# Kernel tuning notes

Measured on AMD Instinct MI355X. Metric: run time of the kernel, lower is better.

The kernel has to match this reference:

```python
import jax, jax.numpy as jnp
import numpy as np

N_HEADS = 4
D_K = 64

def setup_inputs() -> dict:
    key = jax.random.key(0)
    k1, k2, k3 = jax.random.split(key, 3)
    B, C, H, W = 16, 256, 32, 32
    x = jax.random.normal(k1, (B, C, H, W), dtype=jnp.float32)
    # Linear(C, 3*n_heads*d_k) stored as [in, out] for x @ W
    w_proj = jax.random.normal(k2, (C, 3 * N_HEADS * D_K), dtype=jnp.float32) * (1.0 / np.sqrt(C))
    b_proj = jnp.zeros((3 * N_HEADS * D_K,), dtype=jnp.float32)
    w_out = jax.random.normal(k3, (N_HEADS * D_K, C), dtype=jnp.float32) * (1.0 / np.sqrt(N_HEADS * D_K))
    b_out = jnp.zeros((C,), dtype=jnp.float32)
    return {"x": x, "w_proj": w_proj, "b_proj": b_proj, "w_out": w_out, "b_out": b_out}

def reference(x, w_proj, b_proj, w_out, b_out):
    B, C, H, W = x.shape
    S = H * W
    scale = D_K ** -0.5
    xs = x.reshape(B, C, S).transpose(0, 2, 1)            # [B, S, C]
    qkv = (xs @ w_proj + b_proj).reshape(B, S, N_HEADS, 3 * D_K)
    q, k, v = jnp.split(qkv, 3, axis=3)                    # each [B, S, H, dk]
    attn = jnp.einsum('bihd,bjhd->bijh', q, k) * scale     # [B, S, S, heads]
    attn = jax.nn.softmax(attn, axis=2)
    o = jnp.einsum('bijh,bjhd->bihd', attn, v)             # [B, S, heads, dk]
    o = o.reshape(B, S, N_HEADS * D_K)
    res = o @ w_out + b_out + xs                           # [B, S, C]
    return res.transpose(0, 2, 1).reshape(B, C, H, W)
```

## Files before the change

### kernel.cpp

```cpp
#include <hip/hip_runtime.h>
#include <math.h>

#define B_  16
#define C_  256
#define S_  1024
#define NH  4
#define DK  64
#define P3  768
#define ND  256

typedef unsigned short u16;
typedef unsigned int   u32;
typedef float  f32x4  __attribute__((ext_vector_type(4)));
typedef short  bf16x8 __attribute__((ext_vector_type(8)));

#define MFMA16(a, b, c) __builtin_amdgcn_mfma_f32_16x16x32_bf16(a, b, c, 0, 0, 0)

#define QSCALE 0.1803368801111137f

__device__ __forceinline__ u16 f2bf(float f) {
    union { float f; u32 u; } x; x.f = f;
    u32 r = x.u + 0x7fffu + ((x.u >> 16) & 1u);
    return (u16)(r >> 16);
}

__device__ __forceinline__ void stage16(const u16* g, u16* l) {
    __builtin_amdgcn_global_load_lds(
        (const __attribute__((address_space(1))) void*)g,
        (__attribute__((address_space(3))) void*)l, 16, 0, 0);
}

__global__ __launch_bounds__(256) void transpose_cvt(
    const float* __restrict__ src, u16* __restrict__ dst, int R, int Cc)
{
    __shared__ float T[64][65];
    const int tid = threadIdx.x;
    const int c0 = blockIdx.x * 64, r0 = blockIdx.y * 64, z = blockIdx.z;
    src += (size_t)z * R * Cc;
    dst += (size_t)z * R * Cc;

    const int l64 = tid & 63, rr0 = tid >> 6;
    #pragma unroll
    for (int t = 0; t < 16; ++t) {
        int rr = rr0 + t * 4;
        T[rr][l64] = src[(size_t)(r0 + rr) * Cc + c0 + l64];
    }
    __syncthreads();
    const int rp = tid & 31;
    const int cb = tid >> 5;
    #pragma unroll
    for (int t = 0; t < 8; ++t) {
        int c = cb + t * 8;
        u32 lo = f2bf(T[2 * rp][c]);
        u32 hi = f2bf(T[2 * rp + 1][c]);
        *(u32*)&dst[(size_t)(c0 + c) * R + r0 + 2 * rp] = lo | (hi << 16);
    }
}

__global__ __launch_bounds__(256) void transpose_w(
    const float* __restrict__ wp, u16* __restrict__ wpT,
    const float* __restrict__ wo, u16* __restrict__ woT)
{
    const int z = blockIdx.z;
    const int Cc = z ? 256 : 768;
    if ((int)blockIdx.x * 64 >= Cc) return;
    const float* src = z ? wo : wp;
    u16* dst = z ? woT : wpT;
    const int R = 256;

    __shared__ float T[64][65];
    const int tid = threadIdx.x;
    const int c0 = blockIdx.x * 64, r0 = blockIdx.y * 64;

    const int l64 = tid & 63, rr0 = tid >> 6;
    #pragma unroll
    for (int t = 0; t < 16; ++t) {
        int rr = rr0 + t * 4;
        T[rr][l64] = src[(size_t)(r0 + rr) * Cc + c0 + l64];
    }
    __syncthreads();
    const int rp = tid & 31;
    const int cb = tid >> 5;
    #pragma unroll
    for (int t = 0; t < 8; ++t) {
        int c = cb + t * 8;
        u32 lo = f2bf(T[2 * rp][c]);
        u32 hi = f2bf(T[2 * rp + 1][c]);
        *(u32*)&dst[(size_t)(c0 + c) * R + r0 + 2 * rp] = lo | (hi << 16);
    }
}

__global__ __launch_bounds__(256) void qkv_mfma(
    const u16* __restrict__ xt, const u16* __restrict__ wpT,
    const float* __restrict__ bp, u16* __restrict__ qo,
    u16* __restrict__ ko, u16* __restrict__ vo)
{
    __shared__ __align__(16) u16 SM[24576];
    u16* As = SM;
    u16* Bs = SM + 16384;

    const int tid = threadIdx.x;
    const int w = tid >> 6, lane = tid & 63;
    const int n_ = lane & 15, quad = lane >> 4;
    const int n0 = blockIdx.x * 64, s0 = blockIdx.y * 128, b = blockIdx.z;

    const u16* ar0 = xt + ((size_t)b * S_ + s0 + (2 * w + 0) * 16 + n_) * C_ + quad * 8;
    const u16* ar1 = xt + ((size_t)b * S_ + s0 + (2 * w + 1) * 16 + n_) * C_ + quad * 8;
    const u16* br  = wpT + (size_t)(n0 + w * 16 + n_) * C_ + quad * 8;

    f32x4 acc[2][4];
    #pragma unroll
    for (int am = 0; am < 2; ++am)
        #pragma unroll
        for (int nf = 0; nf < 4; ++nf)
            #pragma unroll
            for (int r = 0; r < 4; ++r) acc[am][nf][r] = 0.f;

    #pragma unroll
    for (int kb = 0; kb < 2; ++kb) {
        const int kcb = kb * 128;
        __syncthreads();
        #pragma unroll
        for (int kc = 0; kc < 4; ++kc) {
            stage16(ar0 + kcb + kc * 32, As + ((2 * w + 0) * 4 + kc) * 512);
            stage16(ar1 + kcb + kc * 32, As + ((2 * w + 1) * 4 + kc) * 512);
            stage16(br  + kcb + kc * 32, Bs + (w * 4 + kc) * 512);
        }
        __syncthreads();
        #pragma unroll
        for (int kc = 0; kc < 4; ++kc) {
            bf16x8 af0 = *(const bf16x8*)&As[((2 * w + 0) * 4 + kc) * 512 + lane * 8];
            bf16x8 af1 = *(const bf16x8*)&As[((2 * w + 1) * 4 + kc) * 512 + lane * 8];
            #pragma unroll
            for (int nf = 0; nf < 4; ++nf) {
                bf16x8 bf = *(const bf16x8*)&Bs[(nf * 4 + kc) * 512 + lane * 8];
                acc[0][nf] = MFMA16(af0, bf, acc[0][nf]);
                acc[1][nf] = MFMA16(af1, bf, acc[1][nf]);
            }
        }
    }

    const int hd = n0 / 192, rem = n0 % 192, which = rem / 64;
    const int bh = b * NH + hd;
    float bias[4];
    #pragma unroll
    for (int nf = 0; nf < 4; ++nf) bias[nf] = bp[n0 + nf * 16 + n_];
    const float sc = (which == 0) ? QSCALE : 1.f;

    __syncthreads();
    if (which < 2) {
        u16* Cs = SM;
        #pragma unroll
        for (int am = 0; am < 2; ++am) {
            int row0 = w * 32 + am * 16 + quad * 4;
            #pragma unroll
            for (int nf = 0; nf < 4; ++nf)
                #pragma unroll
                for (int r = 0; r < 4; ++r)
                    Cs[(row0 + r) * 72 + nf * 16 + n_] =
                        f2bf((acc[am][nf][r] + bias[nf]) * sc);
        }
        __syncthreads();
        u16* dst = (which == 0) ? qo : ko;
        #pragma unroll
        for (int t = 0; t < 4; ++t) {
            int ii = tid + t * 256;
            int row = ii >> 3, c8 = (ii & 7) * 8;
            *(bf16x8*)&dst[((size_t)bh * S_ + s0 + row) * DK + c8] =
                *(const bf16x8*)&Cs[row * 72 + c8];
        }
    } else {
        u16* Cs = SM;
        #pragma unroll
        for (int am = 0; am < 2; ++am) {
            int colb = w * 32 + am * 16 + quad * 4;
            #pragma unroll
            for (int nf = 0; nf < 4; ++nf)
                #pragma unroll
                for (int r = 0; r < 4; ++r)
                    Cs[(nf * 16 + n_) * 136 + colb + r] =
                        f2bf(acc[am][nf][r] + bias[nf]);
        }
        __syncthreads();
        #pragma unroll
        for (int t = 0; t < 4; ++t) {
            int ii = tid + t * 256;
            int row = ii >> 4, c8 = (ii & 15) * 8;
            *(bf16x8*)&vo[((size_t)bh * DK + row) * S_ + s0 + c8] =
                *(const bf16x8*)&Cs[row * 136 + c8];
        }
    }
}

__global__ __launch_bounds__(256) void attn_mfma(
    const u16* __restrict__ q, const u16* __restrict__ k,
    const u16* __restrict__ vt, u16* __restrict__ obf)
{
    __shared__ __align__(16) u16 SM[9216];
    u16* Ks = SM;
    u16* Vs = SM + 4096;

    const int tid = threadIdx.x;
    const int w = tid >> 6, lane = tid & 63;
    const int n_ = lane & 15, quad = lane >> 4;
    const int i0 = blockIdx.x * 128;
    const int hd = blockIdx.y, b = blockIdx.z;
    const int bh = b * NH + hd;

    bf16x8 qf[2][2];
    #pragma unroll
    for (int am = 0; am < 2; ++am) {
        const u16* qrow = q + ((size_t)bh * S_ + i0 + w * 32 + am * 16 + n_) * DK;
        qf[am][0] = *(const bf16x8*)&qrow[quad * 8];
        qf[am][1] = *(const bf16x8*)&qrow[32 + quad * 8];
    }

    const int kappa = 32 * (w & 1) + 8 * (n_ >> 2) + 4 * (w >> 1) + (n_ & 3);
    const u16* kbase = k  + ((size_t)bh * S_ + kappa) * DK + quad * 8;
    const u16* vbase = vt + ((size_t)bh * DK + w * 16 + n_) * S_ + quad * 8;

    float lsum[2] = {0.f, 0.f};
    f32x4 oacc[2][4];
    #pragma unroll
    for (int am = 0; am < 2; ++am)
        #pragma unroll
        for (int nd = 0; nd < 4; ++nd)
            #pragma unroll
            for (int r = 0; r < 4; ++r) oacc[am][nd][r] = 0.f;

    for (int jt = 0; jt < S_; jt += 64) {
        __syncthreads();
        stage16(kbase + (size_t)jt * DK,      Ks + w * 1024);
        stage16(kbase + (size_t)jt * DK + 32, Ks + w * 1024 + 512);
        stage16(vbase + jt,                   Vs + w * 1024);
        stage16(vbase + jt + 32,              Vs + w * 1024 + 512);
        __syncthreads();

        f32x4 sb[2][4];
        #pragma unroll
        for (int nb = 0; nb < 4; ++nb) {
            bf16x8 kf0 = *(const bf16x8*)&Ks[nb * 1024 + lane * 8];
            bf16x8 kf1 = *(const bf16x8*)&Ks[nb * 1024 + 512 + lane * 8];
            #pragma unroll
            for (int am = 0; am < 2; ++am) {
                f32x4 a; a[0] = a[1] = a[2] = a[3] = 0.f;
                a = MFMA16(kf0, qf[am][0], a);
                a = MFMA16(kf1, qf[am][1], a);
                sb[am][nb] = a;
            }
        }

        bf16x8 pa[2][2];
        #pragma unroll
        for (int am = 0; am < 2; ++am) {
            u32 tr[4][4];
            #pragma unroll
            for (int nb = 0; nb < 4; ++nb)
                #pragma unroll
                for (int r = 0; r < 4; ++r) {
                    float p = exp2f(sb[am][nb][r]);
                    u32 bits = __float_as_uint(p) & 0xffff0000u;
                    lsum[am] += __uint_as_float(bits);
                    tr[nb][r] = bits;
                }
            union { bf16x8 v; u32 u[4]; } p0, p1;
            p0.u[0] = (tr[0][0] >> 16) | tr[0][1];
            p0.u[1] = (tr[0][2] >> 16) | tr[0][3];
            p0.u[2] = (tr[2][0] >> 16) | tr[2][1];
            p0.u[3] = (tr[2][2] >> 16) | tr[2][3];
            p1.u[0] = (tr[1][0] >> 16) | tr[1][1];
            p1.u[1] = (tr[1][2] >> 16) | tr[1][3];
            p1.u[2] = (tr[3][0] >> 16) | tr[3][1];
            p1.u[3] = (tr[3][2] >> 16) | tr[3][3];
            pa[am][0] = p0.v;
            pa[am][1] = p1.v;
        }

        #pragma unroll
        for (int nd = 0; nd < 4; ++nd) {
            bf16x8 vf0 = *(const bf16x8*)&Vs[nd * 1024 + lane * 8];
            bf16x8 vf1 = *(const bf16x8*)&Vs[nd * 1024 + 512 + lane * 8];
            #pragma unroll
            for (int am = 0; am < 2; ++am) {
                oacc[am][nd] = MFMA16(vf0, pa[am][0], oacc[am][nd]);
                oacc[am][nd] = MFMA16(vf1, pa[am][1], oacc[am][nd]);
            }
        }
    }

    float inv[2];
    #pragma unroll
    for (int am = 0; am < 2; ++am) {
        float s = lsum[am];
        s += __shfl_xor(s, 16);
        s += __shfl_xor(s, 32);
        inv[am] = 1.f / s;
    }

    __syncthreads();
    u16* eb = SM + w * 2304;
    #pragma unroll
    for (int am = 0; am < 2; ++am)
        #pragma unroll
        for (int nd = 0; nd < 4; ++nd) {
            uint2 uv;
            uv.x = (u32)f2bf(oacc[am][nd][0] * inv[am]) |
                   ((u32)f2bf(oacc[am][nd][1] * inv[am]) << 16);
            uv.y = (u32)f2bf(oacc[am][nd][2] * inv[am]) |
                   ((u32)f2bf(oacc[am][nd][3] * inv[am]) << 16);
            *(uint2*)&eb[(am * 16 + n_) * 72 + nd * 16 + quad * 4] = uv;
        }
    __syncthreads();
    #pragma unroll
    for (int t = 0; t < 4; ++t) {
        int ii = lane + t * 64;
        int row = ii >> 3, c8 = (ii & 7) * 8;
        *(bf16x8*)&obf[((size_t)b * S_ + i0 + w * 32 + row) * ND + hd * DK + c8] =
            *(const bf16x8*)&eb[row * 72 + c8];
    }
}

__global__ __launch_bounds__(256) void out_proj_mfma(
    const u16* __restrict__ obf, const u16* __restrict__ woT,
    const float* __restrict__ bo, const float* __restrict__ x,
    float* __restrict__ out)
{
    __shared__ __align__(16) u16 SM[24576];
    u16* Bs = SM;
    u16* As = SM + 16384;

    const int tid = threadIdx.x;
    const int w = tid >> 6, lane = tid & 63;
    const int n_ = lane & 15, quad = lane >> 4;
    const int c0 = blockIdx.x * 64, s0 = blockIdx.y * 128, b = blockIdx.z;

    const u16* ar  = woT + (size_t)(c0 + w * 16 + n_) * ND + quad * 8;
    const u16* br0 = obf + ((size_t)b * S_ + s0 + (2 * w + 0) * 16 + n_) * ND + quad * 8;
    const u16* br1 = obf + ((size_t)b * S_ + s0 + (2 * w + 1) * 16 + n_) * ND + quad * 8;

    f32x4 acc[2][4];
    #pragma unroll
    for (int nf = 0; nf < 2; ++nf)
        #pragma unroll
        for (int mb = 0; mb < 4; ++mb)
            #pragma unroll
            for (int r = 0; r < 4; ++r) acc[nf][mb][r] = 0.f;

    #pragma unroll
    for (int kb = 0; kb < 2; ++kb) {
        const int kcb = kb * 128;
        __syncthreads();
        #pragma unroll
        for (int kc = 0; kc < 4; ++kc) {
            stage16(ar  + kcb + kc * 32, As + (w * 4 + kc) * 512);
            stage16(br0 + kcb + kc * 32, Bs + ((2 * w + 0) * 4 + kc) * 512);
            stage16(br1 + kcb + kc * 32, Bs + ((2 * w + 1) * 4 + kc) * 512);
        }
        __syncthreads();
        #pragma unroll
        for (int kc = 0; kc < 4; ++kc) {
            bf16x8 bf0 = *(const bf16x8*)&Bs[((2 * w + 0) * 4 + kc) * 512 + lane * 8];
            bf16x8 bf1 = *(const bf16x8*)&Bs[((2 * w + 1) * 4 + kc) * 512 + lane * 8];
            #pragma unroll
            for (int mb = 0; mb < 4; ++mb) {
                bf16x8 af = *(const bf16x8*)&As[(mb * 4 + kc) * 512 + lane * 8];
                acc[0][mb] = MFMA16(af, bf0, acc[0][mb]);
                acc[1][mb] = MFMA16(af, bf1, acc[1][mb]);
            }
        }
    }

    #pragma unroll
    for (int mb = 0; mb < 4; ++mb)
        #pragma unroll
        for (int r = 0; r < 4; ++r) {
            int c = c0 + mb * 16 + quad * 4 + r;
            float bias = bo[c];
            #pragma unroll
            for (int nf = 0; nf < 2; ++nf) {
                size_t idx = ((size_t)b * C_ + c) * S_ + s0 + w * 32 + nf * 16 + n_;
                out[idx] = acc[nf][mb][r] + bias + x[idx];
            }
        }
}

extern "C" void kernel_launch(void* const* d_in, const int* in_sizes, int n_in,
                              void* d_out, int out_size, void* d_ws, size_t ws_size,
                              hipStream_t stream) {
    const float* x  = (const float*)d_in[0];
    const float* wp = (const float*)d_in[1];
    const float* bp = (const float*)d_in[2];
    const float* wo = (const float*)d_in[3];
    const float* bo = (const float*)d_in[4];
    float* out = (float*)d_out;

    const size_t QKV_E = (size_t)B_ * NH * S_ * DK;
    u16* q   = (u16*)d_ws;
    u16* kk  = q   + QKV_E;
    u16* vtp = kk  + QKV_E;
    u16* obf = vtp + QKV_E;
    u16* xt  = obf + (size_t)B_ * S_ * ND;
    u16* wpT = xt  + (size_t)B_ * S_ * C_;
    u16* woT = wpT + (size_t)P3 * C_;

    transpose_cvt<<<dim3(S_ / 64, C_ / 64, B_), 256, 0, stream>>>(x, xt, C_, S_);
    transpose_w  <<<dim3(12, 4, 2),             256, 0, stream>>>(wp, wpT, wo, woT);
    qkv_mfma     <<<dim3(P3 / 64, S_ / 128, B_), 256, 0, stream>>>(xt, wpT, bp, q, kk, vtp);
    attn_mfma    <<<dim3(S_ / 128, NH, B_),      256, 0, stream>>>(q, kk, vtp, obf);
    out_proj_mfma<<<dim3(C_ / 64, S_ / 128, B_), 256, 0, stream>>>(obf, woT, bo, x, out);
}
```

Before: 148.3 us.

## Remap blocks to XCDs for L2 locality and double attention key tile

The three GEMM and attention kernels now run on a flattened 1D grid. Block indices are remapped so that consecutive blocks on the same XCD (id & 7) share the same batch/head or sequence region, which is meant to improve L2 reuse of K/V and activations across the MI355X chiplets. The attention kernel also processes 128 keys per iteration instead of 64, with doubled LDS staging. This halves the number of barrier and sync rounds per block and lengthens the MFMA chains, at the cost of more registers and shared memory.

```diff
diff --git a/kernel.cpp b/kernel.cpp
--- a/kernel.cpp
+++ b/kernel.cpp
@@ -102,7 +102,12 @@
     const int tid = threadIdx.x;
     const int w = tid >> 6, lane = tid & 63;
     const int n_ = lane & 15, quad = lane >> 4;
-    const int n0 = blockIdx.x * 64, s0 = blockIdx.y * 128, b = blockIdx.z;
+
+    const int id = blockIdx.x;
+    const int xcd = id & 7, g = id >> 3;
+    const int n0 = (g % 12) * 64;
+    const int sb = xcd * 16 + g / 12;
+    const int s0 = (sb & 7) * 128, b = sb >> 3;
 
     const u16* ar0 = xt + ((size_t)b * S_ + s0 + (2 * w + 0) * 16 + n_) * C_ + quad * 8;
     const u16* ar1 = xt + ((size_t)b * S_ + s0 + (2 * w + 1) * 16 + n_) * C_ + quad * 8;
@@ -196,16 +201,19 @@
     const u16* __restrict__ q, const u16* __restrict__ k,
     const u16* __restrict__ vt, u16* __restrict__ obf)
 {
-    __shared__ __align__(16) u16 SM[9216];
+    __shared__ __align__(16) u16 SM[16384];
     u16* Ks = SM;
-    u16* Vs = SM + 4096;
+    u16* Vs = SM + 8192;
 
     const int tid = threadIdx.x;
     const int w = tid >> 6, lane = tid & 63;
     const int n_ = lane & 15, quad = lane >> 4;
-    const int i0 = blockIdx.x * 128;
-    const int hd = blockIdx.y, b = blockIdx.z;
-    const int bh = b * NH + hd;
+
+    const int id = blockIdx.x;
+    const int xcd = id & 7, g = id >> 3;
+    const int i0 = (g % 8) * 128;
+    const int bh = xcd * 8 + g / 8;
+    const int hd = bh & 3, b = bh >> 2;
 
     bf16x8 qf[2][2];
     #pragma unroll
@@ -215,9 +223,10 @@
         qf[am][1] = *(const bf16x8*)&qrow[32 + quad * 8];
     }
 
-    const int kappa = 32 * (w & 1) + 8 * (n_ >> 2) + 4 * (w >> 1) + (n_ & 3);
-    const u16* kbase = k  + ((size_t)bh * S_ + kappa) * DK + quad * 8;
-    const u16* vbase = vt + ((size_t)bh * DK + w * 16 + n_) * S_ + quad * 8;
+    const int k0 = 32 * w + 8 * (n_ >> 2) + (n_ & 3);
+    const u16* kb0 = k + ((size_t)bh * S_ + k0) * DK + quad * 8;
+    const u16* kb1 = kb0 + 4 * DK;
+    const u16* vb  = vt + ((size_t)bh * DK + w * 16 + n_) * S_ + quad * 8;
 
     float lsum[2] = {0.f, 0.f};
     f32x4 oacc[2][4];
@@ -228,17 +237,20 @@
             #pragma unroll
             for (int r = 0; r < 4; ++r) oacc[am][nd][r] = 0.f;
 
-    for (int jt = 0; jt < S_; jt += 64) {
-        __syncthreads();
-        stage16(kbase + (size_t)jt * DK,      Ks + w * 1024);
-        stage16(kbase + (size_t)jt * DK + 32, Ks + w * 1024 + 512);
-        stage16(vbase + jt,                   Vs + w * 1024);
-        stage16(vbase + jt + 32,              Vs + w * 1024 + 512);
-        __syncthreads();
-
-        f32x4 sb[2][4];
-        #pragma unroll
-        for (int nb = 0; nb < 4; ++nb) {
+    for (int jt = 0; jt < S_; jt += 128) {
+        __syncthreads();
+        stage16(kb0 + (size_t)jt * DK,      Ks + (2 * w + 0) * 1024);
+        stage16(kb0 + (size_t)jt * DK + 32, Ks + (2 * w + 0) * 1024 + 512);
+        stage16(kb1 + (size_t)jt * DK,      Ks + (2 * w + 1) * 1024);
+        stage16(kb1 + (size_t)jt * DK + 32, Ks + (2 * w + 1) * 1024 + 512);
+        #pragma unroll
+        for (int mf = 0; mf < 4; ++mf)
+            stage16(vb + jt + mf * 32, Vs + (w * 4 + mf) * 512);
+        __syncthreads();
+
+        f32x4 sb[2][8];
+        #pragma unroll
+        for (int nb = 0; nb < 8; ++nb) {
             bf16x8 kf0 = *(const bf16x8*)&Ks[nb * 1024 + lane * 8];
             bf16x8 kf1 = *(const bf16x8*)&Ks[nb * 1024 + 512 + lane * 8];
             #pragma unroll
@@ -250,12 +262,12 @@
             }
         }
 
-        bf16x8 pa[2][2];
+        bf16x8 pa[2][4];
         #pragma unroll
         for (int am = 0; am < 2; ++am) {
-            u32 tr[4][4];
-            #pragma unroll
-            for (int nb = 0; nb < 4; ++nb)
+            u32 tr[8][4];
+            #pragma unroll
+            for (int nb = 0; nb < 8; ++nb)
                 #pragma unroll
                 for (int r = 0; r < 4; ++r) {
                     float p = exp2f(sb[am][nb][r]);
@@ -263,29 +275,26 @@
                     lsum[am] += __uint_as_float(bits);
                     tr[nb][r] = bits;
                 }
-            union { bf16x8 v; u32 u[4]; } p0, p1;
-            p0.u[0] = (tr[0][0] >> 16) | tr[0][1];
-            p0.u[1] = (tr[0][2] >> 16) | tr[0][3];
-            p0.u[2] = (tr[2][0] >> 16) | tr[2][1];
-            p0.u[3] = (tr[2][2] >> 16) | tr[2][3];
-            p1.u[0] = (tr[1][0] >> 16) | tr[1][1];
-            p1.u[1] = (tr[1][2] >> 16) | tr[1][3];
-            p1.u[2] = (tr[3][0] >> 16) | tr[3][1];
-            p1.u[3] = (tr[3][2] >> 16) | tr[3][3];
-            pa[am][0] = p0.v;
-            pa[am][1] = p1.v;
-        }
-
-        #pragma unroll
-        for (int nd = 0; nd < 4; ++nd) {
-            bf16x8 vf0 = *(const bf16x8*)&Vs[nd * 1024 + lane * 8];
-            bf16x8 vf1 = *(const bf16x8*)&Vs[nd * 1024 + 512 + lane * 8];
-            #pragma unroll
-            for (int am = 0; am < 2; ++am) {
-                oacc[am][nd] = MFMA16(vf0, pa[am][0], oacc[am][nd]);
-                oacc[am][nd] = MFMA16(vf1, pa[am][1], oacc[am][nd]);
-            }
-        }
+            #pragma unroll
+            for (int mf = 0; mf < 4; ++mf) {
+                union { bf16x8 v; u32 u[4]; } pk;
+                pk.u[0] = (tr[2 * mf][0] >> 16) | tr[2 * mf][1];
+                pk.u[1] = (tr[2 * mf][2] >> 16) | tr[2 * mf][3];
+                pk.u[2] = (tr[2 * mf + 1][0] >> 16) | tr[2 * mf + 1][1];
+                pk.u[3] = (tr[2 * mf + 1][2] >> 16) | tr[2 * mf + 1][3];
+                pa[am][mf] = pk.v;
+            }
+        }
+
+        #pragma unroll
+        for (int nd = 0; nd < 4; ++nd)
+            #pragma unroll
+            for (int mf = 0; mf < 4; ++mf) {
+                bf16x8 vf = *(const bf16x8*)&Vs[(nd * 4 + mf) * 512 + lane * 8];
+                #pragma unroll
+                for (int am = 0; am < 2; ++am)
+                    oacc[am][nd] = MFMA16(vf, pa[am][mf], oacc[am][nd]);
+            }
     }
 
     float inv[2];
@@ -332,7 +341,12 @@
     const int tid = threadIdx.x;
     const int w = tid >> 6, lane = tid & 63;
     const int n_ = lane & 15, quad = lane >> 4;
-    const int c0 = blockIdx.x * 64, s0 = blockIdx.y * 128, b = blockIdx.z;
+
+    const int id = blockIdx.x;
+    const int xcd = id & 7, g = id >> 3;
+    const int c0 = (g % 4) * 64;
+    const int sbi = xcd * 16 + g / 4;
+    const int s0 = (sbi & 7) * 128, b = sbi >> 3;
 
     const u16* ar  = woT + (size_t)(c0 + w * 16 + n_) * ND + quad * 8;
     const u16* br0 = obf + ((size_t)b * S_ + s0 + (2 * w + 0) * 16 + n_) * ND + quad * 8;
@@ -405,7 +419,7 @@
 
     transpose_cvt<<<dim3(S_ / 64, C_ / 64, B_), 256, 0, stream>>>(x, xt, C_, S_);
     transpose_w  <<<dim3(12, 4, 2),             256, 0, stream>>>(wp, wpT, wo, woT);
-    qkv_mfma     <<<dim3(P3 / 64, S_ / 128, B_), 256, 0, stream>>>(xt, wpT, bp, q, kk, vtp);
-    attn_mfma    <<<dim3(S_ / 128, NH, B_),      256, 0, stream>>>(q, kk, vtp, obf);
-    out_proj_mfma<<<dim3(C_ / 64, S_ / 128, B_), 256, 0, stream>>>(obf, woT, bo, x, out);
-}
+    qkv_mfma     <<<dim3(1536), 256, 0, stream>>>(xt, wpT, bp, q, kk, vtp);
+    attn_mfma    <<<dim3(512),  256, 0, stream>>>(q, kk, vtp, obf);
+    out_proj_mfma<<<dim3(512),  256, 0, stream>>>(obf, woT, bo, x, out);
+}
```

After: 150.5 us. Within noise of the previous version (+1.5%).
